# Performance work log

Measured on AMD Instinct MI355X. Metric: run time of the kernel, lower is better.

Reference implementation:

```python
import jax, jax.numpy as jnp
import numpy as np

NE, NPER = 100000, 50000        # empresa / persona node counts
D_EMP, D_PER = 64, 32           # raw feature dims
H, OUT = 128, 64                # hidden_channels, out_channels
E_EE, E_PE, E_EP = 1600000, 800000, 800000
NEG_SLOPE = 0.2                 # GATConv leaky_relu slope


def setup_inputs() -> dict:
    key = jax.random.key(0)
    ks = jax.random.split(key, 40)

    def w(k, fi, fo):
        return jax.random.normal(k, (fi, fo), jnp.float32) / jnp.sqrt(jnp.float32(fi))

    def b(k, n):
        return jax.random.normal(k, (n,), jnp.float32) * 0.02

    return {
        "x_emp": jax.random.normal(ks[0], (NE, D_EMP), jnp.float32),
        "x_per": jax.random.normal(ks[1], (NPER, D_PER), jnp.float32),
        "ee_src": jax.random.randint(ks[2], (E_EE,), 0, NE, jnp.int32),
        "ee_dst": jax.random.randint(ks[3], (E_EE,), 0, NE, jnp.int32),
        "pe_src": jax.random.randint(ks[4], (E_PE,), 0, NPER, jnp.int32),
        "pe_dst": jax.random.randint(ks[5], (E_PE,), 0, NE, jnp.int32),
        "ep_src": jax.random.randint(ks[6], (E_EP,), 0, NE, jnp.int32),
        "ep_dst": jax.random.randint(ks[7], (E_EP,), 0, NPER, jnp.int32),
        # per-node-type input projections
        "lin_emp_w": w(ks[8], D_EMP, H), "lin_emp_b": b(ks[9], H),
        "lin_per_w": w(ks[10], D_PER, H), "lin_per_b": b(ks[11], H),
        # conv1: SAGEConv per edge type (H -> H)
        "s1_ee_Wl": w(ks[12], H, H), "s1_ee_bl": b(ks[13], H), "s1_ee_Wr": w(ks[14], H, H),
        "s1_pe_Wl": w(ks[15], H, H), "s1_pe_bl": b(ks[16], H), "s1_pe_Wr": w(ks[17], H, H),
        "s1_ep_Wl": w(ks[18], H, H), "s1_ep_bl": b(ks[19], H), "s1_ep_Wr": w(ks[20], H, H),
        # conv2: GATConv on empresa->empresa (H -> OUT, heads=1)
        "gat_Wsrc": w(ks[21], H, OUT), "gat_Wdst": w(ks[22], H, OUT),
        "gat_asrc": b(ks[23], OUT), "gat_adst": b(ks[24], OUT), "gat_b": b(ks[25], OUT),
        # conv2: SAGEConv on remaining edge types (H -> OUT)
        "s2_pe_Wl": w(ks[26], H, OUT), "s2_pe_bl": b(ks[27], OUT), "s2_pe_Wr": w(ks[28], H, OUT),
        "s2_ep_Wl": w(ks[29], H, OUT), "s2_ep_bl": b(ks[30], OUT), "s2_ep_Wr": w(ks[31], H, OUT),
    }


def _sage(h_src, h_dst, src, dst, Wl, bl, Wr, n_dst):
    # SAGEConv: mean-aggregate neighbor features, then lin_l(agg) + lin_r(x_dst)
    agg = jax.ops.segment_sum(h_src[src], dst, num_segments=n_dst)
    cnt = jax.ops.segment_sum(jnp.ones((src.shape[0], 1), h_src.dtype), dst,
                              num_segments=n_dst)
    mean = agg / jnp.maximum(cnt, 1.0)  # isolated nodes -> 0 (PyG mean behavior)
    return mean @ Wl + bl + h_dst @ Wr


def _gat(h, src, dst, Wsrc, Wdst, asrc, adst, bias, n):
    # GATConv, heads=1, no self loops: edge-softmax attention over dst neighborhoods
    zs = h @ Wsrc                                   # [n, OUT]
    zd = h @ Wdst
    e = (zs @ asrc)[src] + (zd @ adst)[dst]         # [E] attention logits
    e = jnp.where(e > 0, e, NEG_SLOPE * e)          # leaky_relu(0.2)
    m = jax.ops.segment_max(e, dst, num_segments=n)
    ex = jnp.exp(e - m[dst])
    den = jax.ops.segment_sum(ex, dst, num_segments=n)
    alpha = ex / den[dst]                           # softmax per dst node
    out = jax.ops.segment_sum(zs[src] * alpha[:, None], dst, num_segments=n)
    return out + bias


def reference(x_emp, x_per, ee_src, ee_dst, pe_src, pe_dst, ep_src, ep_dst,
              lin_emp_w, lin_emp_b, lin_per_w, lin_per_b,
              s1_ee_Wl, s1_ee_bl, s1_ee_Wr,
              s1_pe_Wl, s1_pe_bl, s1_pe_Wr,
              s1_ep_Wl, s1_ep_bl, s1_ep_Wr,
              gat_Wsrc, gat_Wdst, gat_asrc, gat_adst, gat_b,
              s2_pe_Wl, s2_pe_bl, s2_pe_Wr,
              s2_ep_Wl, s2_ep_bl, s2_ep_Wr):
    # per-node-type input Linear + relu
    h_emp = jax.nn.relu(x_emp @ lin_emp_w + lin_emp_b)
    h_per = jax.nn.relu(x_per @ lin_per_w + lin_per_b)

    # conv1: HeteroConv of SAGEConvs, aggr='sum' across relations per dst type
    emp1 = (_sage(h_emp, h_emp, ee_src, ee_dst, s1_ee_Wl, s1_ee_bl, s1_ee_Wr, NE)
            + _sage(h_per, h_emp, pe_src, pe_dst, s1_pe_Wl, s1_pe_bl, s1_pe_Wr, NE))
    per1 = _sage(h_emp, h_per, ep_src, ep_dst, s1_ep_Wl, s1_ep_bl, s1_ep_Wr, NPER)
    emp1 = jax.nn.relu(emp1)
    per1 = jax.nn.relu(per1)

    # conv2: GAT on empresa->empresa, SAGE elsewhere, sum across relations
    emp2 = (_gat(emp1, ee_src, ee_dst, gat_Wsrc, gat_Wdst, gat_asrc, gat_adst, gat_b, NE)
            + _sage(per1, emp1, pe_src, pe_dst, s2_pe_Wl, s2_pe_bl, s2_pe_Wr, NE))
    per2 = _sage(emp1, per1, ep_src, ep_dst, s2_ep_Wl, s2_ep_bl, s2_ep_Wr, NPER)
    return emp2, per2
```

## Files before the change

### kernel.cpp

```cpp
#include <hip/hip_runtime.h>
#include <cstdint>

#define NE_N   100000
#define NPER_N 50000
#define HD     128
#define OUTD   64
#define NEE    1600000
#define NPE    800000
#define NEP    800000

static inline int ceil_div(long long a, long long b){ return (int)((a + b - 1)/b); }

__device__ __forceinline__ float4 ld4(const float* p){ return *reinterpret_cast<const float4*>(p); }
__device__ __forceinline__ void st4(float* p, float4 v){ *reinterpret_cast<float4*>(p) = v; }
__device__ __forceinline__ uint16_t f2b(float f){
    uint32_t u = __float_as_uint(f);
    u += 0x7fffu + ((u >> 16) & 1u);
    return (uint16_t)(u >> 16);
}
__device__ __forceinline__ float b2f(uint32_t u){ return __uint_as_float(u << 16); }

typedef short v8s __attribute__((ext_vector_type(8)));
typedef float v4f __attribute__((ext_vector_type(4)));

struct Seg { const uint16_t* W; const float* b; void* C; int ldw; int ldc; int mode; };
struct Segs { Seg s[6]; };

template<int K>
__global__ __launch_bounds__(256)
void gemm_mfma(const uint16_t* __restrict__ A, int N, Segs segs)
{
    constexpr int NKS  = K / 32;
    constexpr int PADK = K + 8;
    __shared__ __align__(16) uint16_t Wt[64 * PADK];

    Seg sg = segs.s[blockIdx.y];

    const int t = threadIdx.x;
    for (int i = t; i < K*64; i += 256){
        int k = i >> 6, c = i & 63;
        Wt[c*PADK + k] = sg.W[(size_t)k*sg.ldw + c];
    }
    __syncthreads();

    const int lane = t & 63, wid = t >> 6;
    const int l16 = lane & 15, lg = lane >> 4;
    const int rowbase = blockIdx.x*256 + wid*64;

    v4f acc[4][4];
#pragma unroll
    for (int i=0;i<4;i++)
#pragma unroll
        for (int j=0;j<4;j++) acc[i][j] = (v4f){0.f,0.f,0.f,0.f};

#pragma unroll
    for (int ks=0; ks<NKS; ks++){
        const int koff = ks*32 + lg*8;
        v8s a[4], b[4];
#pragma unroll
        for (int rt=0;rt<4;rt++){
            int r = rowbase + rt*16 + l16; if (r > N-1) r = N-1;
            a[rt] = *reinterpret_cast<const v8s*>(&A[(size_t)r*K + koff]);
        }
#pragma unroll
        for (int ct=0;ct<4;ct++)
            b[ct] = *reinterpret_cast<const v8s*>(&Wt[(ct*16 + l16)*PADK + koff]);
#pragma unroll
        for (int rt=0;rt<4;rt++)
#pragma unroll
            for (int ct=0;ct<4;ct++)
                acc[rt][ct] = __builtin_amdgcn_mfma_f32_16x16x32_bf16(a[rt], b[ct], acc[rt][ct], 0, 0, 0);
    }

    const int mode = sg.mode, ldc = sg.ldc;
    float bias[4];
    if (mode != 1){
#pragma unroll
        for (int ct=0;ct<4;ct++) bias[ct] = sg.b[ct*16 + l16];
    }
#pragma unroll
    for (int rt=0;rt<4;rt++){
#pragma unroll
        for (int rg=0;rg<4;rg++){
            int r = rowbase + rt*16 + lg*4 + rg;
            if (r < N){
#pragma unroll
                for (int ct=0;ct<4;ct++){
                    float v = acc[rt][ct][rg];
                    int c = ct*16 + l16;
                    if (mode == 0)
                        ((float*)sg.C)[(size_t)r*ldc + c] = v + bias[ct];
                    else if (mode == 1)
                        ((uint16_t*)sg.C)[(size_t)r*ldc + c] = f2b(v);
                    else
                        ((uint16_t*)sg.C)[(size_t)r*ldc + c] = f2b(fmaxf(v + bias[ct], 0.f));
                }
            }
        }
    }
}

__global__ void count_all(const int* __restrict__ ee, const int* __restrict__ pe,
                          const int* __restrict__ ep, int* __restrict__ cnt){
    int i = blockIdx.x*blockDim.x + threadIdx.x;
    if (i < NEE) atomicAdd(&cnt[ee[i]], 1);
    else if (i < NEE+NPE) atomicAdd(&cnt[100000 + pe[i-NEE]], 1);
    else if (i < NEE+NPE+NEP) atomicAdd(&cnt[200000 + ep[i-NEE-NPE]], 1);
}
__global__ __launch_bounds__(256)
void scan_block3(const int* __restrict__ cnt_all, int* __restrict__ ee_off,
                 int* __restrict__ pe_off, int* __restrict__ ep_off,
                 int* __restrict__ partial){
    int r = blockIdx.y;
    const int* cnt = cnt_all + (r==0 ? 0 : (r==1 ? 100000 : 200000));
    int* off = (r==0) ? ee_off : (r==1 ? pe_off : ep_off);
    int n = (r==2) ? NPER_N : NE_N;
    int* part = partial + r*128;

    __shared__ int sh[256];
    int t = threadIdx.x;
    int base = blockIdx.x*1024 + t*4;
    int v0 = (base  <n)?cnt[base  ]:0;
    int v1 = (base+1<n)?cnt[base+1]:0;
    int v2 = (base+2<n)?cnt[base+2]:0;
    int v3 = (base+3<n)?cnt[base+3]:0;
    int tsum = v0+v1+v2+v3;
    sh[t]=tsum; __syncthreads();
    for (int d=1; d<256; d<<=1){
        int x = (t>=d)? sh[t-d] : 0;
        __syncthreads();
        sh[t] += x;
        __syncthreads();
    }
    int ex = sh[t]-tsum;
    if (base  <n) off[base  ]=ex;
    if (base+1<n) off[base+1]=ex+v0;
    if (base+2<n) off[base+2]=ex+v0+v1;
    if (base+3<n) off[base+3]=ex+v0+v1+v2;
    if (t==255) part[blockIdx.x]=sh[255];
}
__global__ void scan_partial3(int* __restrict__ partial){
    int r = blockIdx.x;
    if (threadIdx.x != 0) return;
    int n = (r==2) ? NPER_N : NE_N;
    int nb = (n + 1023) >> 10;
    int* p = partial + r*128;
    int run = 0;
    for (int i=0;i<nb;i++){ int v=p[i]; p[i]=run; run+=v; }
}
__global__ void add_base3(int* __restrict__ ee_off, int* __restrict__ pe_off,
                          int* __restrict__ ep_off, const int* __restrict__ partial){
    int i = blockIdx.x*blockDim.x + threadIdx.x;
    if (i <= NE_N){
        if (i < NE_N) ee_off[i] += partial[i>>10];
        else ee_off[NE_N] = NEE;
    } else if (i <= 2*NE_N + 1){
        int k = i - (NE_N+1);
        if (k < NE_N) pe_off[k] += partial[128 + (k>>10)];
        else pe_off[NE_N] = NPE;
    } else {
        int k = i - 2*(NE_N+1);
        if (k < NPER_N) ep_off[k] += partial[256 + (k>>10)];
        else if (k == NPER_N) ep_off[NPER_N] = NEP;
    }
}
__global__ void fill_all(const int* __restrict__ ee_src, const int* __restrict__ ee_dst,
                         const int* __restrict__ pe_src, const int* __restrict__ pe_dst,
                         const int* __restrict__ ep_src, const int* __restrict__ ep_dst,
                         const int* __restrict__ ee_off, const int* __restrict__ pe_off,
                         const int* __restrict__ ep_off, int* __restrict__ cnt_all,
                         int* __restrict__ ee_csr, int* __restrict__ pe_csr,
                         int* __restrict__ ep_csr){
    int i = blockIdx.x*blockDim.x + threadIdx.x;
    if (i < NEE){
        int d = ee_dst[i];
        int old = atomicAdd(&cnt_all[d], -1);
        ee_csr[ee_off[d] + old - 1] = ee_src[i];
    } else if (i < NEE+NPE){
        int k = i - NEE;
        int d = pe_dst[k];
        int old = atomicAdd(&cnt_all[100000 + d], -1);
        pe_csr[pe_off[d] + old - 1] = pe_src[k];
    } else if (i < NEE+NPE+NEP){
        int k = i - NEE - NPE;
        int d = ep_dst[k];
        int old = atomicAdd(&cnt_all[200000 + d], -1);
        ep_csr[ep_off[d] + old - 1] = ep_src[k];
    }
}

__global__ __launch_bounds__(256)
void agg_emp1(const uint16_t* __restrict__ proj_ee, const uint16_t* __restrict__ proj_pe,
              const int* __restrict__ ee_off, const int* __restrict__ ee_csr,
              const int* __restrict__ pe_off, const int* __restrict__ pe_csr,
              const float* __restrict__ emp1f, uint16_t* __restrict__ emp1b){
    int w    = (blockIdx.x*blockDim.x + threadIdx.x) >> 6;
    int lane = threadIdx.x & 63;
    if (w >= NE_N) return;
    int grp = lane >> 4, l16 = lane & 15;

    float a[8] = {0,0,0,0,0,0,0,0};
    int b = ee_off[w], e = ee_off[w+1];
    int dee = e - b;
    for (int cb=b; cb<e; cb+=64){
        int j = cb + lane;
        int s = (j<e) ? ee_csr[j] : -1;
        int lim = e - cb; if (lim > 64) lim = 64;
        int iters = (lim + 3) >> 2;
        for (int k=0;k<iters;k++){
            int sg = __shfl(s, k*4 + grp, 64);
            if (sg >= 0){
                uint4 u = *reinterpret_cast<const uint4*>(&proj_ee[(size_t)sg*128 + l16*8]);
                a[0]+=b2f(u.x&0xffffu); a[1]+=b2f(u.x>>16);
                a[2]+=b2f(u.y&0xffffu); a[3]+=b2f(u.y>>16);
                a[4]+=b2f(u.z&0xffffu); a[5]+=b2f(u.z>>16);
                a[6]+=b2f(u.w&0xffffu); a[7]+=b2f(u.w>>16);
            }
        }
    }
    float c[8] = {0,0,0,0,0,0,0,0};
    b = pe_off[w]; e = pe_off[w+1];
    int dpe = e - b;
    for (int cb=b; cb<e; cb+=64){
        int j = cb + lane;
        int s = (j<e) ? pe_csr[j] : -1;
        int lim = e - cb; if (lim > 64) lim = 64;
        int iters = (lim + 3) >> 2;
        for (int k=0;k<iters;k++){
            int sg = __shfl(s, k*4 + grp, 64);
            if (sg >= 0){
                uint4 u = *reinterpret_cast<const uint4*>(&proj_pe[(size_t)sg*128 + l16*8]);
                c[0]+=b2f(u.x&0xffffu); c[1]+=b2f(u.x>>16);
                c[2]+=b2f(u.y&0xffffu); c[3]+=b2f(u.y>>16);
                c[4]+=b2f(u.z&0xffffu); c[5]+=b2f(u.z>>16);
                c[6]+=b2f(u.w&0xffffu); c[7]+=b2f(u.w>>16);
            }
        }
    }
#pragma unroll
    for (int f=0;f<8;f++){
        a[f] += __shfl_xor(a[f],16,64); a[f] += __shfl_xor(a[f],32,64);
        c[f] += __shfl_xor(c[f],16,64); c[f] += __shfl_xor(c[f],32,64);
    }
    if (grp == 0){
        float s1f = 1.f/fmaxf((float)dee,1.f);
        float s2f = 1.f/fmaxf((float)dpe,1.f);
        float4 e0 = ld4(&emp1f[(size_t)w*128 + l16*8]);
        float4 e1 = ld4(&emp1f[(size_t)w*128 + l16*8 + 4]);
        float o[8];
        o[0]=fmaxf(e0.x + a[0]*s1f + c[0]*s2f, 0.f);
        o[1]=fmaxf(e0.y + a[1]*s1f + c[1]*s2f, 0.f);
        o[2]=fmaxf(e0.z + a[2]*s1f + c[2]*s2f, 0.f);
        o[3]=fmaxf(e0.w + a[3]*s1f + c[3]*s2f, 0.f);
        o[4]=fmaxf(e1.x + a[4]*s1f + c[4]*s2f, 0.f);
        o[5]=fmaxf(e1.y + a[5]*s1f + c[5]*s2f, 0.f);
        o[6]=fmaxf(e1.z + a[6]*s1f + c[6]*s2f, 0.f);
        o[7]=fmaxf(e1.w + a[7]*s1f + c[7]*s2f, 0.f);
        uint4 pk;
        pk.x = (uint32_t)f2b(o[0]) | ((uint32_t)f2b(o[1])<<16);
        pk.y = (uint32_t)f2b(o[2]) | ((uint32_t)f2b(o[3])<<16);
        pk.z = (uint32_t)f2b(o[4]) | ((uint32_t)f2b(o[5])<<16);
        pk.w = (uint32_t)f2b(o[6]) | ((uint32_t)f2b(o[7])<<16);
        *reinterpret_cast<uint4*>(&emp1b[(size_t)w*128 + l16*8]) = pk;
    }
}
__global__ __launch_bounds__(256)
void agg_per1(const uint16_t* __restrict__ proj_ep,
              const int* __restrict__ ep_off, const int* __restrict__ ep_csr,
              const float* __restrict__ per1f, uint16_t* __restrict__ per1b){
    int w    = (blockIdx.x*blockDim.x + threadIdx.x) >> 6;
    int lane = threadIdx.x & 63;
    if (w >= NPER_N) return;
    int grp = lane >> 4, l16 = lane & 15;

    float a[8] = {0,0,0,0,0,0,0,0};
    int b = ep_off[w], e = ep_off[w+1];
    int deg = e - b;
    for (int cb=b; cb<e; cb+=64){
        int j = cb + lane;
        int s = (j<e) ? ep_csr[j] : -1;
        int lim = e - cb; if (lim > 64) lim = 64;
        int iters = (lim + 3) >> 2;
        for (int k=0;k<iters;k++){
            int sg = __shfl(s, k*4 + grp, 64);
            if (sg >= 0){
                uint4 u = *reinterpret_cast<const uint4*>(&proj_ep[(size_t)sg*128 + l16*8]);
                a[0]+=b2f(u.x&0xffffu); a[1]+=b2f(u.x>>16);
                a[2]+=b2f(u.y&0xffffu); a[3]+=b2f(u.y>>16);
                a[4]+=b2f(u.z&0xffffu); a[5]+=b2f(u.z>>16);
                a[6]+=b2f(u.w&0xffffu); a[7]+=b2f(u.w>>16);
            }
        }
    }
#pragma unroll
    for (int f=0;f<8;f++){
        a[f] += __shfl_xor(a[f],16,64); a[f] += __shfl_xor(a[f],32,64);
    }
    if (grp == 0){
        float s1f = 1.f/fmaxf((float)deg,1.f);
        float4 e0 = ld4(&per1f[(size_t)w*128 + l16*8]);
        float4 e1 = ld4(&per1f[(size_t)w*128 + l16*8 + 4]);
        float o[8];
        o[0]=fmaxf(e0.x + a[0]*s1f, 0.f); o[1]=fmaxf(e0.y + a[1]*s1f, 0.f);
        o[2]=fmaxf(e0.z + a[2]*s1f, 0.f); o[3]=fmaxf(e0.w + a[3]*s1f, 0.f);
        o[4]=fmaxf(e1.x + a[4]*s1f, 0.f); o[5]=fmaxf(e1.y + a[5]*s1f, 0.f);
        o[6]=fmaxf(e1.z + a[6]*s1f, 0.f); o[7]=fmaxf(e1.w + a[7]*s1f, 0.f);
        uint4 pk;
        pk.x = (uint32_t)f2b(o[0]) | ((uint32_t)f2b(o[1])<<16);
        pk.y = (uint32_t)f2b(o[2]) | ((uint32_t)f2b(o[3])<<16);
        pk.z = (uint32_t)f2b(o[4]) | ((uint32_t)f2b(o[5])<<16);
        pk.w = (uint32_t)f2b(o[6]) | ((uint32_t)f2b(o[7])<<16);
        *reinterpret_cast<uint4*>(&per1b[(size_t)w*128 + l16*8]) = pk;
    }
}
__global__ __launch_bounds__(256)
void agg_per2(const uint16_t* __restrict__ p2ep,
              const int* __restrict__ ep_off, const int* __restrict__ ep_csr,
              float* __restrict__ out){
    int w    = (blockIdx.x*blockDim.x + threadIdx.x) >> 6;
    int lane = threadIdx.x & 63;
    if (w >= NPER_N) return;
    int grp = lane >> 4, l16 = lane & 15;

    float a[4] = {0,0,0,0};
    int b = ep_off[w], e = ep_off[w+1];
    int deg = e - b;
    for (int cb=b; cb<e; cb+=64){
        int j = cb + lane;
        int s = (j<e) ? ep_csr[j] : -1;
        int lim = e - cb; if (lim > 64) lim = 64;
        int iters = (lim + 3) >> 2;
        for (int k=0;k<iters;k++){
            int sg = __shfl(s, k*4 + grp, 64);
            if (sg >= 0){
                uint2 u = *reinterpret_cast<const uint2*>(&p2ep[(size_t)sg*64 + l16*4]);
                a[0]+=b2f(u.x&0xffffu); a[1]+=b2f(u.x>>16);
                a[2]+=b2f(u.y&0xffffu); a[3]+=b2f(u.y>>16);
            }
        }
    }
#pragma unroll
    for (int f=0;f<4;f++){
        a[f] += __shfl_xor(a[f],16,64); a[f] += __shfl_xor(a[f],32,64);
    }
    if (grp == 0){
        float s1f = 1.f/fmaxf((float)deg,1.f);
        float4 o4 = ld4(&out[(size_t)w*64 + l16*4]);
        o4.x += a[0]*s1f; o4.y += a[1]*s1f; o4.z += a[2]*s1f; o4.w += a[3]*s1f;
        st4(&out[(size_t)w*64 + l16*4], o4);
    }
}
__global__ __launch_bounds__(256)
void gat_sage_emp2(const int* __restrict__ ee_off, const int* __restrict__ ee_csr,
                   const int* __restrict__ pe_off, const int* __restrict__ pe_csr,
                   const float* __restrict__ as, const float* __restrict__ ad,
                   const uint16_t* __restrict__ zs, const uint16_t* __restrict__ p2pe,
                   float* __restrict__ out){
    int w    = (blockIdx.x*blockDim.x + threadIdx.x) >> 6;
    int lane = threadIdx.x & 63;
    if (w >= NE_N) return;
    int grp = lane >> 4, l16 = lane & 15;

    float g[4] = {0,0,0,0};
    float invden = 0.f;
    int b = ee_off[w], e = ee_off[w+1];
    if (e > b){
        float add = ad[w];
        float m = -INFINITY;
        for (int j=b+lane; j<e; j+=64){
            float ev = as[ee_csr[j]] + add;
            ev = ev > 0.f ? ev : 0.2f*ev;
            m = fmaxf(m, ev);
        }
        for (int o=32;o;o>>=1) m = fmaxf(m, __shfl_xor(m,o,64));

        float den = 0.f;
        for (int cb=b; cb<e; cb+=64){
            int j = cb + lane;
            int s = 0; float ex = 0.f;
            if (j < e){
                s = ee_csr[j];
                float ev = as[s] + add;
                ev = ev > 0.f ? ev : 0.2f*ev;
                ex = expf(ev - m);
            }
            den += ex;
            int lim = e - cb; if (lim > 64) lim = 64;
            int iters = (lim + 3) >> 2;
            for (int k=0;k<iters;k++){
                int   sg = __shfl(s,  k*4 + grp, 64);
                float ag = __shfl(ex, k*4 + grp, 64);
                uint2 u = *reinterpret_cast<const uint2*>(&zs[(size_t)sg*64 + l16*4]);
                g[0] += ag*b2f(u.x&0xffffu); g[1] += ag*b2f(u.x>>16);
                g[2] += ag*b2f(u.y&0xffffu); g[3] += ag*b2f(u.y>>16);
            }
        }
        for (int o=32;o;o>>=1) den += __shfl_xor(den,o,64);
        invden = 1.f/den;
    }

    float p[4] = {0,0,0,0};
    b = pe_off[w]; e = pe_off[w+1];
    int deg = e - b;
    for (int cb=b; cb<e; cb+=64){
        int j = cb + lane;
        int s = (j<e) ? pe_csr[j] : -1;
        int lim = e - cb; if (lim > 64) lim = 64;
        int iters = (lim + 3) >> 2;
        for (int k=0;k<iters;k++){
            int sg = __shfl(s, k*4 + grp, 64);
            if (sg >= 0){
                uint2 u = *reinterpret_cast<const uint2*>(&p2pe[(size_t)sg*64 + l16*4]);
                p[0]+=b2f(u.x&0xffffu); p[1]+=b2f(u.x>>16);
                p[2]+=b2f(u.y&0xffffu); p[3]+=b2f(u.y>>16);
            }
        }
    }
#pragma unroll
    for (int f=0;f<4;f++){
        g[f] += __shfl_xor(g[f],16,64); g[f] += __shfl_xor(g[f],32,64);
        p[f] += __shfl_xor(p[f],16,64); p[f] += __shfl_xor(p[f],32,64);
    }
    if (grp == 0){
        float s2f = 1.f/fmaxf((float)deg,1.f);
        float4 o4 = ld4(&out[(size_t)w*64 + l16*4]);
        o4.x += g[0]*invden + p[0]*s2f;
        o4.y += g[1]*invden + p[1]*s2f;
        o4.z += g[2]*invden + p[2]*s2f;
        o4.w += g[3]*invden + p[3]*s2f;
        st4(&out[(size_t)w*64 + l16*4], o4);
    }
}

__global__ void rowdots(const uint16_t* __restrict__ ZS, const uint16_t* __restrict__ E1,
                        const float* __restrict__ wa, const float* __restrict__ wv,
                        float* __restrict__ a_s, float* __restrict__ a_d){
    int wid  = (blockIdx.x*blockDim.x + threadIdx.x) >> 6;
    int lane = threadIdx.x & 63;
    if (wid < NE_N){
        float v = b2f((uint32_t)ZS[(size_t)wid*64 + lane])*wa[lane];
        for (int o=32;o;o>>=1) v += __shfl_xor(v,o,64);
        if (lane==0) a_s[wid]=v;
    } else if (wid < 2*NE_N){
        int k = wid - NE_N;
        float v = b2f((uint32_t)E1[(size_t)k*128 + lane])*wv[lane]
                + b2f((uint32_t)E1[(size_t)k*128 + 64 + lane])*wv[64+lane];
        for (int o=32;o;o>>=1) v += __shfl_xor(v,o,64);
        if (lane==0) a_d[k]=v;
    }
}

constexpr int WB_WSUM   = 0;
constexpr int WB_EEWL   = 16384;
constexpr int WB_EPWL   = 32768;
constexpr int WB_PEWL   = 49152;
constexpr int WB_EPWR1  = 65536;
constexpr int WB_LINE   = 81920;
constexpr int WB_LINP   = 90112;
constexpr int WB_GATW   = 94208;
constexpr int WB_S2EPWL = 102400;
constexpr int WB_S2PEWR = 110592;
constexpr int WB_S2PEWL = 118784;
constexpr int WB_S2EPWR = 126976;

__global__ void prep(const float* Wr_ee, const float* Wr_pe,
                     const float* ee_Wl, const float* ep_Wl, const float* pe_Wl, const float* ep_Wr,
                     const float* line_w, const float* linp_w,
                     const float* gatW, const float* s2epWl, const float* s2peWr,
                     const float* s2peWl, const float* s2epWr,
                     const float* bl_ee, const float* bl_pe,
                     const float* s2_pe_bl, const float* gat_b,
                     const float* Wdst, const float* adst,
                     uint16_t* wb, float* bsum1, float* b2sum, float* vvec)
{
    int j = blockIdx.x, t = threadIdx.x;
    if (j == 12){
        if (t < HD){
            bsum1[t] = bl_ee[t] + bl_pe[t];
            float s = 0.f;
            for (int c=0;c<OUTD;c++) s += Wdst[t*OUTD + c]*adst[c];
            vvec[t] = s;
        }
        if (t < OUTD) b2sum[t] = s2_pe_bl[t] + gat_b[t];
        return;
    }
    if (j == 0){
        for (int i=t; i<16384; i+=256) wb[WB_WSUM + i] = f2b(Wr_ee[i] + Wr_pe[i]);
        return;
    }
    const float* src; uint16_t* dst; int n;
    switch(j){
        case 1:  src=ee_Wl;  dst=wb+WB_EEWL;   n=16384; break;
        case 2:  src=ep_Wl;  dst=wb+WB_EPWL;   n=16384; break;
        case 3:  src=pe_Wl;  dst=wb+WB_PEWL;   n=16384; break;
        case 4:  src=ep_Wr;  dst=wb+WB_EPWR1;  n=16384; break;
        case 5:  src=line_w; dst=wb+WB_LINE;   n=8192;  break;
        case 6:  src=linp_w; dst=wb+WB_LINP;   n=4096;  break;
        case 7:  src=gatW;   dst=wb+WB_GATW;   n=8192;  break;
        case 8:  src=s2epWl; dst=wb+WB_S2EPWL; n=8192;  break;
        case 9:  src=s2peWr; dst=wb+WB_S2PEWR; n=8192;  break;
        case 10: src=s2peWl; dst=wb+WB_S2PEWL; n=8192;  break;
        default: src=s2epWr; dst=wb+WB_S2EPWR; n=8192;  break;
    }
    for (int i=t; i<n; i+=256) dst[i] = f2b(src[i]);
}

__global__ void convx(const float* __restrict__ xe, const float* __restrict__ xp,
                      uint16_t* __restrict__ be, uint16_t* __restrict__ bp){
    const int NE4 = NE_N*64/4, NP4 = NPER_N*32/4;
    int i = blockIdx.x*blockDim.x + threadIdx.x;
    if (i < NE4){
        float4 v = ld4(xe + (size_t)i*4);
        uint2 o;
        o.x = (uint32_t)f2b(v.x) | ((uint32_t)f2b(v.y) << 16);
        o.y = (uint32_t)f2b(v.z) | ((uint32_t)f2b(v.w) << 16);
        *reinterpret_cast<uint2*>(&be[(size_t)i*4]) = o;
    } else if (i < NE4 + NP4){
        int k = i - NE4;
        float4 v = ld4(xp + (size_t)k*4);
        uint2 o;
        o.x = (uint32_t)f2b(v.x) | ((uint32_t)f2b(v.y) << 16);
        o.y = (uint32_t)f2b(v.z) | ((uint32_t)f2b(v.w) << 16);
        *reinterpret_cast<uint2*>(&bp[(size_t)k*4]) = o;
    }
}

constexpr size_t OFF_R0 = 0;
constexpr size_t OFF_R1 = 3200000;
constexpr size_t OFF_R2 = 4800000;
constexpr size_t OFF_R3 = 11200000;
constexpr size_t OFF_R4 = 14400000;
constexpr size_t OFF_R5 = 27200000;
constexpr size_t OFF_R6 = 33600000;
constexpr size_t OFF_R7 = 40000000;
constexpr size_t OFF_R8 = 43200000;
constexpr size_t OFF_AS = 49600000;
constexpr size_t OFF_AD = 49700000;
constexpr size_t OFF_WB = 49800000;
constexpr size_t OFF_BS1= 49900000;
constexpr size_t OFF_BS2= 49900128;
constexpr size_t OFF_VV = 49900192;
constexpr size_t OFF_CNT    = 50000000;
constexpr size_t OFF_EE_OFF = 50250000;
constexpr size_t OFF_PE_OFF = 50350008;
constexpr size_t OFF_EP_OFF = 50450016;
constexpr size_t OFF_PART   = 50500024;
constexpr size_t OFF_EE_CSR = 50500416;
constexpr size_t OFF_PE_CSR = 52100416;
constexpr size_t OFF_EP_CSR = 52900416;

extern "C" void kernel_launch(void* const* d_in, const int* in_sizes, int n_in,
                              void* d_out, int out_size, void* d_ws, size_t ws_size,
                              hipStream_t stream)
{
    const float* x_emp = (const float*)d_in[0];
    const float* x_per = (const float*)d_in[1];
    const int* ee_src = (const int*)d_in[2];
    const int* ee_dst = (const int*)d_in[3];
    const int* pe_src = (const int*)d_in[4];
    const int* pe_dst = (const int*)d_in[5];
    const int* ep_src = (const int*)d_in[6];
    const int* ep_dst = (const int*)d_in[7];
    const float* lin_emp_w=(const float*)d_in[8],  *lin_emp_b=(const float*)d_in[9];
    const float* lin_per_w=(const float*)d_in[10], *lin_per_b=(const float*)d_in[11];
    const float* s1_ee_Wl=(const float*)d_in[12], *s1_ee_bl=(const float*)d_in[13], *s1_ee_Wr=(const float*)d_in[14];
    const float* s1_pe_Wl=(const float*)d_in[15], *s1_pe_bl=(const float*)d_in[16], *s1_pe_Wr=(const float*)d_in[17];
    const float* s1_ep_Wl=(const float*)d_in[18], *s1_ep_bl=(const float*)d_in[19], *s1_ep_Wr=(const float*)d_in[20];
    const float* gat_Wsrc=(const float*)d_in[21], *gat_Wdst=(const float*)d_in[22];
    const float* gat_asrc=(const float*)d_in[23], *gat_adst=(const float*)d_in[24], *gat_b=(const float*)d_in[25];
    const float* s2_pe_Wl=(const float*)d_in[26], *s2_pe_bl=(const float*)d_in[27], *s2_pe_Wr=(const float*)d_in[28];
    const float* s2_ep_Wl=(const float*)d_in[29], *s2_ep_bl=(const float*)d_in[30], *s2_ep_Wr=(const float*)d_in[31];

    float* ws = (float*)d_ws;
    int*   wi = (int*)d_ws;
    float* out_emp = (float*)d_out;
    float* out_per = out_emp + (size_t)NE_N*OUTD;

    uint16_t* xbe     = (uint16_t*)(ws + OFF_R0);
    uint16_t* zsB     = (uint16_t*)(ws + OFF_R0);
    uint16_t* xbp     = (uint16_t*)(ws + OFF_R1);
    uint16_t* p2peB   = (uint16_t*)(ws + OFF_R1);
    uint16_t* h_empB  = (uint16_t*)(ws + OFF_R2);
    uint16_t* emp1B   = (uint16_t*)(ws + OFF_R2);
    uint16_t* h_perB  = (uint16_t*)(ws + OFF_R3);
    uint16_t* per1B   = (uint16_t*)(ws + OFF_R3);
    float*    emp1F   = ws + OFF_R4;
    uint16_t* p2epB   = (uint16_t*)(ws + OFF_R4);
    float*    per1F   = ws + OFF_R5;
    uint16_t* proj_eeB= (uint16_t*)(ws + OFF_R6);
    uint16_t* proj_peB= (uint16_t*)(ws + OFF_R7);
    uint16_t* proj_epB= (uint16_t*)(ws + OFF_R8);
    float* a_s   = ws + OFF_AS;
    float* a_d   = ws + OFF_AD;
    uint16_t* WB = (uint16_t*)(ws + OFF_WB);
    float* bsum1 = ws + OFF_BS1;
    float* b2sum = ws + OFF_BS2;
    float* vvec  = ws + OFF_VV;

    int* cnt_all = wi + OFF_CNT;
    int* ee_off = wi + OFF_EE_OFF; int* ee_csr = wi + OFF_EE_CSR;
    int* pe_off = wi + OFF_PE_OFF; int* pe_csr = wi + OFF_PE_CSR;
    int* ep_off = wi + OFF_EP_OFF; int* ep_csr = wi + OFF_EP_CSR;
    int* part   = wi + OFF_PART;

    const int GE = ceil_div(NE_N,256), GP = ceil_div(NPER_N,256);

    hipMemsetAsync(cnt_all, 0, 250000*sizeof(int), stream);

    prep<<<13,256,0,stream>>>(s1_ee_Wr, s1_pe_Wr, s1_ee_Wl, s1_ep_Wl, s1_pe_Wl, s1_ep_Wr,
                              lin_emp_w, lin_per_w,
                              gat_Wsrc, s2_ep_Wl, s2_pe_Wr, s2_pe_Wl, s2_ep_Wr,
                              s1_ee_bl, s1_pe_bl, s2_pe_bl, gat_b, gat_Wdst, gat_adst,
                              WB, bsum1, b2sum, vvec);
    convx<<<ceil_div(NE_N*64/4 + NPER_N*32/4, 256),256,0,stream>>>(x_emp, x_per, xbe, xbp);

    count_all<<<ceil_div(NEE+NPE+NEP,256),256,0,stream>>>(ee_dst, pe_dst, ep_dst, cnt_all);
    scan_block3<<<dim3(ceil_div(NE_N,1024),3),256,0,stream>>>(cnt_all, ee_off, pe_off, ep_off, part);
    scan_partial3<<<3,64,0,stream>>>(part);
    add_base3<<<ceil_div(2*(NE_N+1)+NPER_N+1,256),256,0,stream>>>(ee_off, pe_off, ep_off, part);
    fill_all<<<ceil_div(NEE+NPE+NEP,256),256,0,stream>>>(ee_src, ee_dst, pe_src, pe_dst, ep_src, ep_dst,
                                                         ee_off, pe_off, ep_off, cnt_all,
                                                         ee_csr, pe_csr, ep_csr);

    {
        Segs g{};
        g.s[0] = Seg{WB+WB_LINE,    lin_emp_b,    (void*)h_empB,      128,128,2};
        g.s[1] = Seg{WB+WB_LINE+64, lin_emp_b+64, (void*)(h_empB+64), 128,128,2};
        g.s[2]=g.s[0]; g.s[3]=g.s[0]; g.s[4]=g.s[0]; g.s[5]=g.s[0];
        gemm_mfma<64><<<dim3(GE,2),256,0,stream>>>(xbe, NE_N, g);
    }
    {
        Segs g{};
        g.s[0] = Seg{WB+WB_LINP,    lin_per_b,    (void*)h_perB,      128,128,2};
        g.s[1] = Seg{WB+WB_LINP+64, lin_per_b+64, (void*)(h_perB+64), 128,128,2};
        g.s[2]=g.s[0]; g.s[3]=g.s[0]; g.s[4]=g.s[0]; g.s[5]=g.s[0];
        gemm_mfma<32><<<dim3(GP,2),256,0,stream>>>(xbp, NPER_N, g);
    }

    {
        Segs g{};
        g.s[0] = Seg{WB+WB_WSUM,    bsum1,    (void*)emp1F,        128,128,0};
        g.s[1] = Seg{WB+WB_WSUM+64, bsum1+64, (void*)(emp1F+64),   128,128,0};
        g.s[2] = Seg{WB+WB_EEWL,    nullptr,  (void*)proj_eeB,     128,128,1};
        g.s[3] = Seg{WB+WB_EEWL+64, nullptr,  (void*)(proj_eeB+64),128,128,1};
        g.s[4] = Seg{WB+WB_EPWL,    nullptr,  (void*)proj_epB,     128,128,1};
        g.s[5] = Seg{WB+WB_EPWL+64, nullptr,  (void*)(proj_epB+64),128,128,1};
        gemm_mfma<128><<<dim3(GE,6),256,0,stream>>>(h_empB, NE_N, g);
    }
    {
        Segs g{};
        g.s[0] = Seg{WB+WB_PEWL,    nullptr,     (void*)proj_peB,     128,128,1};
        g.s[1] = Seg{WB+WB_PEWL+64, nullptr,     (void*)(proj_peB+64),128,128,1};
        g.s[2] = Seg{WB+WB_EPWR1,   s1_ep_bl,    (void*)per1F,        128,128,0};
        g.s[3] = Seg{WB+WB_EPWR1+64,s1_ep_bl+64, (void*)(per1F+64),   128,128,0};
        g.s[4]=g.s[0]; g.s[5]=g.s[0];
        gemm_mfma<128><<<dim3(GP,4),256,0,stream>>>(h_perB, NPER_N, g);
    }
    agg_emp1<<<ceil_div((long long)NE_N*64,256),256,0,stream>>>(proj_eeB, proj_peB, ee_off, ee_csr, pe_off, pe_csr, emp1F, emp1B);
    agg_per1<<<ceil_div((long long)NPER_N*64,256),256,0,stream>>>(proj_epB, ep_off, ep_csr, per1F, per1B);

    {
        Segs g{};
        g.s[0] = Seg{WB+WB_GATW,   nullptr, (void*)zsB,     64,64,1};
        g.s[1] = Seg{WB+WB_S2EPWL, nullptr, (void*)p2epB,   64,64,1};
        g.s[2] = Seg{WB+WB_S2PEWR, b2sum,   (void*)out_emp, 64,64,0};
        g.s[3]=g.s[0]; g.s[4]=g.s[0]; g.s[5]=g.s[0];
        gemm_mfma<128><<<dim3(GE,3),256,0,stream>>>(emp1B, NE_N, g);
    }
    rowdots<<<ceil_div(2*NE_N,4),256,0,stream>>>(zsB, emp1B, gat_asrc, vvec, a_s, a_d);
    {
        Segs g{};
        g.s[0] = Seg{WB+WB_S2PEWL, nullptr,  (void*)p2peB,   64,64,1};
        g.s[1] = Seg{WB+WB_S2EPWR, s2_ep_bl, (void*)out_per, 64,64,0};
        g.s[2]=g.s[0]; g.s[3]=g.s[0]; g.s[4]=g.s[0]; g.s[5]=g.s[0];
        gemm_mfma<128><<<dim3(GP,2),256,0,stream>>>(per1B, NPER_N, g);
    }

    gat_sage_emp2<<<ceil_div((long long)NE_N*64,256),256,0,stream>>>(ee_off, ee_csr, pe_off, pe_csr, a_s, a_d, zsB, p2peB, out_emp);
    agg_per2<<<ceil_div((long long)NPER_N*64,256),256,0,stream>>>(p2epB, ep_off, ep_csr, out_per);
}
```

Before: 809.3 us.

## Build CSR via two-level bucketed counting sort with per-bucket local scatter

Replaces per-destination global atomic counting, multi-kernel scan and random scatter with a bucketed sort. Edges are binned into 64-destination buckets split across 8 sub-counters, scanned in a single block, scattered as packed (src, local dst) pairs, then each bucket builds its CSR slice using shared-memory atomics. This aims to cut global atomic contention and the uncoalesced scatter into the CSR arrays. The cost is an extra pass over a pairs buffer and a serial single-block scan.

```diff
diff --git a/kernel.cpp b/kernel.cpp
--- a/kernel.cpp
+++ b/kernel.cpp
@@ -8,6 +8,13 @@
 #define NEE    1600000
 #define NPE    800000
 #define NEP    800000
+#define ETOT   (NEE+NPE+NEP)
+
+#define NB_EE  1563
+#define NB_PE  1563
+#define NB_EP  782
+#define NBT    (NB_EE+NB_PE+NB_EP)
+#define NSEG   (NBT*8)
 
 static inline int ceil_div(long long a, long long b){ return (int)((a + b - 1)/b); }
 
@@ -100,92 +107,95 @@
     }
 }
 
-__global__ void count_all(const int* __restrict__ ee, const int* __restrict__ pe,
-                          const int* __restrict__ ep, int* __restrict__ cnt){
-    int i = blockIdx.x*blockDim.x + threadIdx.x;
-    if (i < NEE) atomicAdd(&cnt[ee[i]], 1);
-    else if (i < NEE+NPE) atomicAdd(&cnt[100000 + pe[i-NEE]], 1);
-    else if (i < NEE+NPE+NEP) atomicAdd(&cnt[200000 + ep[i-NEE-NPE]], 1);
+__global__ void bcount(const int* __restrict__ ee_dst, const int* __restrict__ pe_dst,
+                       const int* __restrict__ ep_dst, int* __restrict__ cnt8){
+    int i = blockIdx.x*256 + threadIdx.x;
+    int c = blockIdx.x & 7;
+    int b;
+    if (i < NEE) b = ee_dst[i] >> 6;
+    else if (i < NEE+NPE) b = NB_EE + (pe_dst[i-NEE] >> 6);
+    else b = NB_EE+NB_PE + (ep_dst[i-NEE-NPE] >> 6);
+    atomicAdd(&cnt8[b*8 + c], 1);
 }
 __global__ __launch_bounds__(256)
-void scan_block3(const int* __restrict__ cnt_all, int* __restrict__ ee_off,
-                 int* __restrict__ pe_off, int* __restrict__ ep_off,
-                 int* __restrict__ partial){
-    int r = blockIdx.y;
-    const int* cnt = cnt_all + (r==0 ? 0 : (r==1 ? 100000 : 200000));
-    int* off = (r==0) ? ee_off : (r==1 ? pe_off : ep_off);
-    int n = (r==2) ? NPER_N : NE_N;
-    int* part = partial + r*128;
-
+void bscan(const int* __restrict__ cnt8, int* __restrict__ boff,
+           int* __restrict__ ee_off, int* __restrict__ pe_off, int* __restrict__ ep_off){
     __shared__ int sh[256];
+    const int CH = 123;
     int t = threadIdx.x;
-    int base = blockIdx.x*1024 + t*4;
-    int v0 = (base  <n)?cnt[base  ]:0;
-    int v1 = (base+1<n)?cnt[base+1]:0;
-    int v2 = (base+2<n)?cnt[base+2]:0;
-    int v3 = (base+3<n)?cnt[base+3]:0;
-    int tsum = v0+v1+v2+v3;
-    sh[t]=tsum; __syncthreads();
+    int base = t*CH;
+    int sum = 0;
+#pragma unroll 1
+    for (int k=0;k<CH;k++){
+        int i = base + k;
+        if (i < NSEG) sum += cnt8[i];
+    }
+    sh[t] = sum; __syncthreads();
     for (int d=1; d<256; d<<=1){
         int x = (t>=d)? sh[t-d] : 0;
         __syncthreads();
         sh[t] += x;
         __syncthreads();
     }
-    int ex = sh[t]-tsum;
-    if (base  <n) off[base  ]=ex;
-    if (base+1<n) off[base+1]=ex+v0;
-    if (base+2<n) off[base+2]=ex+v0+v1;
-    if (base+3<n) off[base+3]=ex+v0+v1+v2;
-    if (t==255) part[blockIdx.x]=sh[255];
-}
-__global__ void scan_partial3(int* __restrict__ partial){
-    int r = blockIdx.x;
-    if (threadIdx.x != 0) return;
-    int n = (r==2) ? NPER_N : NE_N;
-    int nb = (n + 1023) >> 10;
-    int* p = partial + r*128;
-    int run = 0;
-    for (int i=0;i<nb;i++){ int v=p[i]; p[i]=run; run+=v; }
-}
-__global__ void add_base3(int* __restrict__ ee_off, int* __restrict__ pe_off,
-                          int* __restrict__ ep_off, const int* __restrict__ partial){
-    int i = blockIdx.x*blockDim.x + threadIdx.x;
-    if (i <= NE_N){
-        if (i < NE_N) ee_off[i] += partial[i>>10];
-        else ee_off[NE_N] = NEE;
-    } else if (i <= 2*NE_N + 1){
-        int k = i - (NE_N+1);
-        if (k < NE_N) pe_off[k] += partial[128 + (k>>10)];
-        else pe_off[NE_N] = NPE;
-    } else {
-        int k = i - 2*(NE_N+1);
-        if (k < NPER_N) ep_off[k] += partial[256 + (k>>10)];
-        else if (k == NPER_N) ep_off[NPER_N] = NEP;
-    }
-}
-__global__ void fill_all(const int* __restrict__ ee_src, const int* __restrict__ ee_dst,
+    int run = sh[t] - sum;
+#pragma unroll 1
+    for (int k=0;k<CH;k++){
+        int i = base + k;
+        if (i < NSEG){ boff[i] = run; run += cnt8[i]; }
+    }
+    if (t == 255) boff[NSEG] = ETOT;
+    if (t == 0){ ee_off[NE_N] = NEE; pe_off[NE_N] = NPE; ep_off[NPER_N] = NEP; }
+}
+__global__ void bscatter(const int* __restrict__ ee_src, const int* __restrict__ ee_dst,
                          const int* __restrict__ pe_src, const int* __restrict__ pe_dst,
                          const int* __restrict__ ep_src, const int* __restrict__ ep_dst,
-                         const int* __restrict__ ee_off, const int* __restrict__ pe_off,
-                         const int* __restrict__ ep_off, int* __restrict__ cnt_all,
-                         int* __restrict__ ee_csr, int* __restrict__ pe_csr,
-                         int* __restrict__ ep_csr){
-    int i = blockIdx.x*blockDim.x + threadIdx.x;
-    if (i < NEE){
-        int d = ee_dst[i];
-        int old = atomicAdd(&cnt_all[d], -1);
-        ee_csr[ee_off[d] + old - 1] = ee_src[i];
-    } else if (i < NEE+NPE){
-        int k = i - NEE;
-        int d = pe_dst[k];
-        int old = atomicAdd(&cnt_all[100000 + d], -1);
-        pe_csr[pe_off[d] + old - 1] = pe_src[k];
-    } else if (i < NEE+NPE+NEP){
-        int k = i - NEE - NPE;
-        int d = ep_dst[k];
-        int old = atomicAdd(&cnt_all[200000 + d], -1);
-        ep_csr[ep_off[d] + old - 1] = ep_src[k];
+                         const int* __restrict__ boff, int* __restrict__ cnt2,
+                         uint32_t* __restrict__ pairs){
+    int i = blockIdx.x*256 + threadIdx.x;
+    int c = blockIdx.x & 7;
+    int b, s, d;
+    if (i < NEE){ d = ee_dst[i]; s = ee_src[i]; b = d >> 6; }
+    else if (i < NEE+NPE){ int k=i-NEE; d = pe_dst[k]; s = pe_src[k]; b = NB_EE + (d >> 6); }
+    else { int k=i-NEE-NPE; d = ep_dst[k]; s = ep_src[k]; b = NB_EE+NB_PE + (d >> 6); }
+    int seg = b*8 + c;
+    int pos = boff[seg] + atomicAdd(&cnt2[seg], 1);
+    pairs[pos] = (uint32_t)s | ((uint32_t)(d & 63) << 20);
+}
+__global__ __launch_bounds__(256)
+void build_csr(const uint32_t* __restrict__ pairs, const int* __restrict__ boff,
+               int* __restrict__ ee_off, int* __restrict__ pe_off, int* __restrict__ ep_off,
+               int* __restrict__ ee_csr, int* __restrict__ pe_csr, int* __restrict__ ep_csr){
+    __shared__ int lcnt[64];
+    __shared__ int loff[64];
+    int b = blockIdx.x, t = threadIdx.x;
+    int pstart = boff[b*8];
+    int pend   = boff[b*8 + 8];
+    int relbase, dst0, n_dst;
+    int* offp; int* csrp;
+    if (b < NB_EE){ relbase = 0; dst0 = b*64; n_dst = NE_N - dst0; offp = ee_off; csrp = ee_csr; }
+    else if (b < NB_EE+NB_PE){ relbase = NEE; dst0 = (b-NB_EE)*64; n_dst = NE_N - dst0; offp = pe_off; csrp = pe_csr; }
+    else { relbase = NEE+NPE; dst0 = (b-NB_EE-NB_PE)*64; n_dst = NPER_N - dst0; offp = ep_off; csrp = ep_csr; }
+    if (n_dst > 64) n_dst = 64;
+    int csr_base = pstart - relbase;
+
+    if (t < 64) lcnt[t] = 0;
+    __syncthreads();
+    for (int i = pstart + t; i < pend; i += 256)
+        atomicAdd(&lcnt[(pairs[i] >> 20) & 63], 1);
+    __syncthreads();
+    if (t == 0){
+        int run = 0;
+        for (int k=0;k<64;k++){ int v = lcnt[k]; loff[k] = run; run += v; }
+    }
+    __syncthreads();
+    if (t < n_dst) offp[dst0 + t] = csr_base + loff[t];
+    if (t < 64) lcnt[t] = loff[t];
+    __syncthreads();
+    for (int i = pstart + t; i < pend; i += 256){
+        uint32_t u = pairs[i];
+        int ld = (u >> 20) & 63;
+        int pos = atomicAdd(&lcnt[ld], 1);
+        csrp[csr_base + pos] = (int)(u & 0xFFFFFu);
     }
 }
 
@@ -540,14 +550,16 @@
 constexpr size_t OFF_BS1= 49900000;
 constexpr size_t OFF_BS2= 49900128;
 constexpr size_t OFF_VV = 49900192;
-constexpr size_t OFF_CNT    = 50000000;
-constexpr size_t OFF_EE_OFF = 50250000;
-constexpr size_t OFF_PE_OFF = 50350008;
-constexpr size_t OFF_EP_OFF = 50450016;
-constexpr size_t OFF_PART   = 50500024;
-constexpr size_t OFF_EE_CSR = 50500416;
-constexpr size_t OFF_PE_CSR = 52100416;
-constexpr size_t OFF_EP_CSR = 52900416;
+constexpr size_t OFF_CNT8   = 50000000;
+constexpr size_t OFF_CNT2   = 50040000;
+constexpr size_t OFF_BOFF   = 50080000;
+constexpr size_t OFF_EE_OFF = 50120000;
+constexpr size_t OFF_PE_OFF = 50220008;
+constexpr size_t OFF_EP_OFF = 50320016;
+constexpr size_t OFF_PAIRS  = 50400000;
+constexpr size_t OFF_EE_CSR = 53600000;
+constexpr size_t OFF_PE_CSR = 55200000;
+constexpr size_t OFF_EP_CSR = 56000000;
 
 extern "C" void kernel_launch(void* const* d_in, const int* in_sizes, int n_in,
                               void* d_out, int out_size, void* d_ws, size_t ws_size,
@@ -597,15 +609,17 @@
     float* b2sum = ws + OFF_BS2;
     float* vvec  = ws + OFF_VV;
 
-    int* cnt_all = wi + OFF_CNT;
+    int* cnt8  = wi + OFF_CNT8;
+    int* cnt2  = wi + OFF_CNT2;
+    int* boff  = wi + OFF_BOFF;
     int* ee_off = wi + OFF_EE_OFF; int* ee_csr = wi + OFF_EE_CSR;
     int* pe_off = wi + OFF_PE_OFF; int* pe_csr = wi + OFF_PE_CSR;
     int* ep_off = wi + OFF_EP_OFF; int* ep_csr = wi + OFF_EP_CSR;
-    int* part   = wi + OFF_PART;
+    uint32_t* pairs = (uint32_t*)(wi + OFF_PAIRS);
 
     const int GE = ceil_div(NE_N,256), GP = ceil_div(NPER_N,256);
 
-    hipMemsetAsync(cnt_all, 0, 250000*sizeof(int), stream);
+    hipMemsetAsync(cnt8, 0, (OFF_CNT2 - OFF_CNT8 + 31264)*sizeof(int), stream);
 
     prep<<<13,256,0,stream>>>(s1_ee_Wr, s1_pe_Wr, s1_ee_Wl, s1_ep_Wl, s1_pe_Wl, s1_ep_Wr,
                               lin_emp_w, lin_per_w,
@@ -614,13 +628,12 @@
                               WB, bsum1, b2sum, vvec);
     convx<<<ceil_div(NE_N*64/4 + NPER_N*32/4, 256),256,0,stream>>>(x_emp, x_per, xbe, xbp);
 
-    count_all<<<ceil_div(NEE+NPE+NEP,256),256,0,stream>>>(ee_dst, pe_dst, ep_dst, cnt_all);
-    scan_block3<<<dim3(ceil_div(NE_N,1024),3),256,0,stream>>>(cnt_all, ee_off, pe_off, ep_off, part);
-    scan_partial3<<<3,64,0,stream>>>(part);
-    add_base3<<<ceil_div(2*(NE_N+1)+NPER_N+1,256),256,0,stream>>>(ee_off, pe_off, ep_off, part);
-    fill_all<<<ceil_div(NEE+NPE+NEP,256),256,0,stream>>>(ee_src, ee_dst, pe_src, pe_dst, ep_src, ep_dst,
-                                                         ee_off, pe_off, ep_off, cnt_all,
-                                                         ee_csr, pe_csr, ep_csr);
+    bcount<<<ETOT/256,256,0,stream>>>(ee_dst, pe_dst, ep_dst, cnt8);
+    bscan<<<1,256,0,stream>>>(cnt8, boff, ee_off, pe_off, ep_off);
+    bscatter<<<ETOT/256,256,0,stream>>>(ee_src, ee_dst, pe_src, pe_dst, ep_src, ep_dst,
+                                        boff, cnt2, pairs);
+    build_csr<<<NBT,256,0,stream>>>(pairs, boff, ee_off, pe_off, ep_off,
+                                    ee_csr, pe_csr, ep_csr);
 
     {
         Segs g{};
@@ -636,7 +649,6 @@
         g.s[2]=g.s[0]; g.s[3]=g.s[0]; g.s[4]=g.s[0]; g.s[5]=g.s[0];
         gemm_mfma<32><<<dim3(GP,2),256,0,stream>>>(xbp, NPER_N, g);
     }
-
     {
         Segs g{};
         g.s[0] = Seg{WB+WB_WSUM,    bsum1,    (void*)emp1F,        128,128,0};
```

Measured after the change: 928.2 us. 14.7% more time.
